# Performance work log

Hardware: AMD Instinct MI355X
Metric: run time of the kernel (lower is better)

Reference implementation:

```python
import jax, jax.numpy as jnp
import numpy as np

def _dct_mat():
    k = np.arange(8)[:, None]
    n = np.arange(8)[None, :]
    norm = np.where(k == 0, np.sqrt(1.0 / 8.0), np.sqrt(2.0 / 8.0))
    return jnp.asarray(norm * np.cos(np.pi / 8.0 * (n + 0.5) * k), jnp.float32)

_LUM = np.array([[16,11,10,16,24,40,51,61],[12,12,14,19,26,58,60,55],[14,13,16,24,40,57,69,56],[14,17,22,29,51,87,80,62],[18,22,37,56,68,109,103,77],[24,35,55,64,81,104,113,92],[49,64,78,87,103,121,120,101],[72,92,95,98,112,100,103,99]], np.float32)
_CHROM = np.array([[17,18,24,47,99,99,99,99],[18,21,26,66,99,99,99,99],[24,26,56,99,99,99,99,99],[47,66,99,99,99,99,99,99],[99,99,99,99,99,99,99,99],[99,99,99,99,99,99,99,99],[99,99,99,99,99,99,99,99],[99,99,99,99,99,99,99,99]], np.float32)

def _qtables(quality):
    q = max(1, min(100, int(quality)))
    scale = 5000.0 / q if q < 50 else 200.0 - 2.0 * q
    tbs = np.stack([_LUM, _CHROM]) * scale
    tbs = np.clip((tbs + 50.0) / 100.0, 1.0, 255.0)
    return jnp.asarray(tbs, jnp.float32)

def _jpeg_forward(img, quality):
    bs, _, oh, ow = img.shape
    x = img * 255.0
    pad_h = (8 - oh % 8) % 8
    pad_w = (8 - ow % 8) % 8
    if pad_h or pad_w:
        x = jnp.pad(x, ((0, 0), (0, 0), (0, pad_h), (0, pad_w)), mode='edge')
    h, w = oh + pad_h, ow + pad_w
    W_ycc = jnp.asarray([[0.299, 0.587, 0.114], [-0.1687, -0.3313, 0.5], [0.5, -0.4187, -0.0813]], jnp.float32)
    b_ycc = jnp.asarray([0.0, 128.0, 128.0], jnp.float32)
    # 1x1 conv colorspace transform
    yuv = jnp.einsum('oc,bchw->bohw', W_ycc, x) + b_ycc[None, :, None, None]
    nb = bs * 3
    hb, wb = h // 8, w // 8
    # unfold(kernel=8, stride=8) == non-overlapping 8x8 blocking, block-row-major
    blocks = yuv.reshape(nb, hb, 8, wb, 8).transpose(0, 1, 3, 2, 4).reshape(nb, hb * wb, 8, 8)
    M = _dct_mat()
    dct = jnp.matmul(M, jnp.matmul(blocks - 128.0, M.T))
    qt = _qtables(quality)
    # faithful to original slicing patches_dct[:bs] / [bs:] over the flattened (b,c) dim
    row = jnp.arange(nb)[:, None, None, None]
    qfull = jnp.where(row < bs, qt[0], qt[1])
    t = dct / qfull
    # straight-through round
    tq = (t + jax.lax.stop_gradient(jnp.round(t) - t)) * qfull
    idct = jnp.matmul(M.T, jnp.matmul(tq, M)) + 128.0
    rec = idct.reshape(nb, hb, wb, 8, 8).transpose(0, 1, 3, 2, 4).reshape(bs, 3, h, w)
    rec = rec - b_ycc[None, :, None, None]
    y, cb, cr = rec[:, 0], rec[:, 1], rec[:, 2]
    r = y + 1.402 * cr
    g = y - 0.34414 * cb - 0.71414 * cr
    b = y + 1.772 * cb
    rgb = jnp.stack([r, g, b], axis=1)[:, :, :oh, :ow]
    return jnp.clip(rgb / 255.0, 0.0, 1.0)

def setup_inputs() -> dict:
    key = jax.random.key(0)
    img = jax.random.uniform(key, (16, 3, 512, 512), dtype=jnp.float32)
    return {"img": img, "quality": 80}

def reference(img, quality):
    return _jpeg_forward(img, quality)
```

## Files before the change

kernel.cpp:

```cpp
#include <hip/hip_runtime.h>
#include <math.h>

#define C1 0.9807852804032304
#define C2 0.9238795325112867
#define C3 0.8314696123025452
#define C4 0.7071067811865476
#define C5 0.5555702330196022
#define C6 0.3826834323650898
#define C7 0.19509032201612825
#define N0 0.35355339059327373

static constexpr double Mc[8][8] = {
 {  N0,      N0,      N0,      N0,      N0,      N0,      N0,      N0    },
 {  .5*C1,   .5*C3,   .5*C5,   .5*C7,  -.5*C7,  -.5*C5,  -.5*C3,  -.5*C1 },
 {  .5*C2,   .5*C6,  -.5*C6,  -.5*C2,  -.5*C2,  -.5*C6,   .5*C6,   .5*C2 },
 {  .5*C3,  -.5*C7,  -.5*C1,  -.5*C5,   .5*C5,   .5*C1,   .5*C7,  -.5*C3 },
 {  .5*C4,  -.5*C4,  -.5*C4,   .5*C4,   .5*C4,  -.5*C4,  -.5*C4,   .5*C4 },
 {  .5*C5,  -.5*C1,   .5*C7,   .5*C3,  -.5*C3,  -.5*C7,   .5*C1,  -.5*C5 },
 {  .5*C6,  -.5*C2,   .5*C2,  -.5*C6,  -.5*C6,   .5*C2,  -.5*C2,   .5*C6 },
 {  .5*C7,  -.5*C5,   .5*C3,  -.5*C1,   .5*C1,  -.5*C3,   .5*C5,  -.5*C7 },
};
#define ROWF(r) {(float)Mc[r][0],(float)Mc[r][1],(float)Mc[r][2],(float)Mc[r][3],\
                 (float)Mc[r][4],(float)Mc[r][5],(float)Mc[r][6],(float)Mc[r][7]}
static constexpr float Mcf[8][8] = {ROWF(0),ROWF(1),ROWF(2),ROWF(3),ROWF(4),ROWF(5),ROWF(6),ROWF(7)};

static __device__ const double LUM_BASE[64] = {
 16,11,10,16,24,40,51,61,
 12,12,14,19,26,58,60,55,
 14,13,16,24,40,57,69,56,
 14,17,22,29,51,87,80,62,
 18,22,37,56,68,109,103,77,
 24,35,55,64,81,104,113,92,
 49,64,78,87,103,121,120,101,
 72,92,95,98,112,100,103,99};
static __device__ const double CHROM_BASE[64] = {
 17,18,24,47,99,99,99,99,
 18,21,26,66,99,99,99,99,
 24,26,56,99,99,99,99,99,
 47,66,99,99,99,99,99,99,
 99,99,99,99,99,99,99,99,
 99,99,99,99,99,99,99,99,
 99,99,99,99,99,99,99,99,
 99,99,99,99,99,99,99,99};

__global__ __launch_bounds__(192, 4) void jpeg_fwd(const float* __restrict__ img,
                                                   const int* __restrict__ quality,
                                                   float* __restrict__ out)
{
    __shared__ double QT[128];
    __shared__ double U[1728];

    const int t   = threadIdx.x;
    const int w   = t >> 6;
    const int l   = t & 63;
    const int blk = l >> 3;
    const int rr  = l & 7;

    const int b    = blockIdx.x >> 9;
    const int rem  = blockIdx.x & 511;
    const int row0 = (rem >> 3) << 3;
    const int col0 = (rem & 7) << 6;

    const size_t plane = 512 * 512;

    const float* p = img + (size_t)(b * 3) * plane + (size_t)(row0 + rr) * 512 + col0 + blk * 8;
    float4 R0 = *(const float4*)(p);
    float4 R1 = *(const float4*)(p + 4);
    float4 G0 = *(const float4*)(p + plane);
    float4 G1 = *(const float4*)(p + plane + 4);
    float4 B0 = *(const float4*)(p + 2 * plane);
    float4 B1 = *(const float4*)(p + 2 * plane + 4);

    {
        int q = quality[0];
        q = q < 1 ? 1 : (q > 100 ? 100 : q);
        double scale = (q < 50) ? (5000.0 / (double)q) : (200.0 - 2.0 * (double)q);
        #pragma unroll
        for (int h = 0; h < 2; ++h) {
            int e = l + (h << 6);
            int tbl = e >> 6, idx = e & 63;
            double base = tbl ? CHROM_BASE[idx] : LUM_BASE[idx];
            double v = (base * scale + 50.0) / 100.0;
            QT[e] = fmin(fmax(v, 1.0), 255.0);
        }
    }

    const double W00 =  0.299,   W01 =  0.587,   W02 =  0.114;
    const double W10 = -0.1687,  W11 = -0.3313,  W12 =  0.5;
    const double W20 =  0.5,     W21 = -0.4187,  W22 = -0.0813;

    float rf[8] = {R0.x, R0.y, R0.z, R0.w, R1.x, R1.y, R1.z, R1.w};
    float gf[8] = {G0.x, G0.y, G0.z, G0.w, G1.x, G1.y, G1.z, G1.w};
    float bf[8] = {B0.x, B0.y, B0.z, B0.w, B1.x, B1.y, B1.z, B1.w};

    double row[8];
    #pragma unroll
    for (int k = 0; k < 8; ++k) {
        double rv = (double)rf[k] * 255.0;
        double gv = (double)gf[k] * 255.0;
        double bv = (double)bf[k] * 255.0;
        double v;
        if (w == 0)      v = W00 * rv + W01 * gv + W02 * bv;
        else if (w == 1) v = W10 * rv + W11 * gv + W12 * bv + 128.0;
        else             v = W20 * rv + W21 * gv + W22 * bv + 128.0;
        row[k] = v - 128.0;
    }

    double y[8];
    #pragma unroll
    for (int c = 0; c < 8; ++c) {
        double s = 0.0;
        #pragma unroll
        for (int k = 0; k < 8; ++k)
            s += row[k] * Mc[c][k];
        y[c] = s;
    }

    {
        double* tb = U + w * 576 + blk * 72 + rr * 9;
        #pragma unroll
        for (int k = 0; k < 8; ++k) tb[k] = y[k];
    }
    double t1[8], qv[8];
    {
        const double* tb = U + w * 576 + blk * 72 + rr;
        #pragma unroll
        for (int k = 0; k < 8; ++k) t1[k] = tb[k * 9];
    }
    const int sel = ((b * 3 + w) < 16) ? 0 : 1;
    #pragma unroll
    for (int j = 0; j < 8; ++j) qv[j] = QT[(sel << 6) + (j << 3) + rr];

    double wq[8];
    #pragma unroll
    for (int j = 0; j < 8; ++j) {
        double s = 0.0;
        #pragma unroll
        for (int k = 0; k < 8; ++k)
            s += t1[k] * Mc[j][k];
        wq[j] = rint(s / qv[j]) * qv[j];
    }

    float wqf[8];
    #pragma unroll
    for (int k = 0; k < 8; ++k) wqf[k] = (float)wq[k];

    float a3[8];
    #pragma unroll
    for (int j = 0; j < 8; ++j) {
        float s = 0.0f;
        #pragma unroll
        for (int k = 0; k < 8; ++k)
            s += wqf[k] * Mcf[k][j];
        a3[j] = s;
    }

    {
        float* tb = (float*)(U + w * 576) + blk * 72 + rr * 9;
        #pragma unroll
        for (int k = 0; k < 8; ++k) tb[k] = a3[k];
    }
    __syncthreads();

    float tY[8], tU[8], tV[8];
    {
        const float* c0 = (float*)(U + 0 * 576) + blk * 72 + rr;
        const float* c1 = (float*)(U + 1 * 576) + blk * 72 + rr;
        const float* c2 = (float*)(U + 2 * 576) + blk * 72 + rr;
        #pragma unroll
        for (int k = 0; k < 8; ++k) {
            tY[k] = c0[k * 9];
            tU[k] = c1[k * 9];
            tV[k] = c2[k * 9];
        }
    }

    float yr[8], ur[8], vr[8];
    #pragma unroll
    for (int j = 0; j < 8; ++j) {
        float sy = 0.0f, su = 0.0f, sv = 0.0f;
        #pragma unroll
        for (int k = 0; k < 8; ++k) {
            sy += tY[k] * Mcf[k][j];
            su += tU[k] * Mcf[k][j];
            sv += tV[k] * Mcf[k][j];
        }
        yr[j] = sy; ur[j] = su; vr[j] = sv;
    }

    float* q0 = out + (size_t)(b * 3 + w) * plane + (size_t)(row0 + rr) * 512 + col0 + blk * 8;
    float o[8];
    #pragma unroll
    for (int k = 0; k < 8; ++k) {
        float yd = yr[k] + 128.0f;
        float v;
        if (w == 0)      v = yd + 1.402f * vr[k];
        else if (w == 1) v = yd - 0.34414f * ur[k] - 0.71414f * vr[k];
        else             v = yd + 1.772f * ur[k];
        o[k] = fminf(fmaxf(v * (1.0f / 255.0f), 0.0f), 1.0f);
    }
    *(float4*)(q0)     = make_float4(o[0], o[1], o[2], o[3]);
    *(float4*)(q0 + 4) = make_float4(o[4], o[5], o[6], o[7]);
}

extern "C" void kernel_launch(void* const* d_in, const int* in_sizes, int n_in,
                              void* d_out, int out_size, void* d_ws, size_t ws_size,
                              hipStream_t stream) {
    const float* img     = (const float*)d_in[0];
    const int*   quality = (const int*)d_in[1];
    float*       out     = (float*)d_out;
    jpeg_fwd<<<8192, 192, 0, stream>>>(img, quality, out);
}
```

Before: 113.0 us.

## Use even/odd DCT symmetry, reciprocal-based quantization, and fold 255 scale

Exploits the even/odd symmetry of the DCT basis to halve the multiply-adds in both forward and inverse 1D transforms. Replaces the FP64 division during quantization with a precomputed reciprocal table plus one FMA correction step. Folds the 255 scaling into the color conversion weights. FP64 arithmetic is the main compute cost, so fewer FP64 ops and no divides should lower ALU time. The risk is small rounding differences at quantization boundaries.

```diff
diff --git a/kernel.cpp b/kernel.cpp
--- a/kernel.cpp
+++ b/kernel.cpp
@@ -48,6 +48,7 @@
                                                    float* __restrict__ out)
 {
     __shared__ double QT[128];
+    __shared__ double RQ[128];
     __shared__ double U[1728];
 
     const int t   = threadIdx.x;
@@ -81,13 +82,15 @@
             int tbl = e >> 6, idx = e & 63;
             double base = tbl ? CHROM_BASE[idx] : LUM_BASE[idx];
             double v = (base * scale + 50.0) / 100.0;
-            QT[e] = fmin(fmax(v, 1.0), 255.0);
-        }
-    }
-
-    const double W00 =  0.299,   W01 =  0.587,   W02 =  0.114;
-    const double W10 = -0.1687,  W11 = -0.3313,  W12 =  0.5;
-    const double W20 =  0.5,     W21 = -0.4187,  W22 = -0.0813;
+            v = fmin(fmax(v, 1.0), 255.0);
+            QT[e] = v;
+            RQ[e] = 1.0 / v;
+        }
+    }
+
+    const double F00 =  0.299 * 255.0,  F01 =  0.587 * 255.0,  F02 =  0.114 * 255.0;
+    const double F10 = -0.1687 * 255.0, F11 = -0.3313 * 255.0, F12 =  0.5 * 255.0;
+    const double F20 =  0.5 * 255.0,    F21 = -0.4187 * 255.0, F22 = -0.0813 * 255.0;
 
     float rf[8] = {R0.x, R0.y, R0.z, R0.w, R1.x, R1.y, R1.z, R1.w};
     float gf[8] = {G0.x, G0.y, G0.z, G0.w, G1.x, G1.y, G1.z, G1.w};
@@ -96,24 +99,34 @@
     double row[8];
     #pragma unroll
     for (int k = 0; k < 8; ++k) {
-        double rv = (double)rf[k] * 255.0;
-        double gv = (double)gf[k] * 255.0;
-        double bv = (double)bf[k] * 255.0;
+        double rv = (double)rf[k];
+        double gv = (double)gf[k];
+        double bv = (double)bf[k];
         double v;
-        if (w == 0)      v = W00 * rv + W01 * gv + W02 * bv;
-        else if (w == 1) v = W10 * rv + W11 * gv + W12 * bv + 128.0;
-        else             v = W20 * rv + W21 * gv + W22 * bv + 128.0;
+        if (w == 0)      v = F00 * rv + F01 * gv + F02 * bv;
+        else if (w == 1) v = F10 * rv + F11 * gv + F12 * bv + 128.0;
+        else             v = F20 * rv + F21 * gv + F22 * bv + 128.0;
         row[k] = v - 128.0;
     }
 
     double y[8];
-    #pragma unroll
-    for (int c = 0; c < 8; ++c) {
-        double s = 0.0;
-        #pragma unroll
-        for (int k = 0; k < 8; ++k)
-            s += row[k] * Mc[c][k];
-        y[c] = s;
+    {
+        double u0[4], v0[4];
+        #pragma unroll
+        for (int k = 0; k < 4; ++k) {
+            u0[k] = row[k] + row[7 - k];
+            v0[k] = row[k] - row[7 - k];
+        }
+        #pragma unroll
+        for (int c = 0; c < 8; c += 2) {
+            double se = 0.0, so = 0.0;
+            #pragma unroll
+            for (int k = 0; k < 4; ++k) {
+                se += u0[k] * Mc[c][k];
+                so += v0[k] * Mc[c + 1][k];
+            }
+            y[c] = se; y[c + 1] = so;
+        }
     }
 
     {
@@ -121,7 +134,7 @@
         #pragma unroll
         for (int k = 0; k < 8; ++k) tb[k] = y[k];
     }
-    double t1[8], qv[8];
+    double t1[8], qv[8], rv8[8];
     {
         const double* tb = U + w * 576 + blk * 72 + rr;
         #pragma unroll
@@ -129,16 +142,42 @@
     }
     const int sel = ((b * 3 + w) < 16) ? 0 : 1;
     #pragma unroll
-    for (int j = 0; j < 8; ++j) qv[j] = QT[(sel << 6) + (j << 3) + rr];
+    for (int j = 0; j < 8; ++j) {
+        qv[j]  = QT[(sel << 6) + (j << 3) + rr];
+        rv8[j] = RQ[(sel << 6) + (j << 3) + rr];
+    }
 
     double wq[8];
-    #pragma unroll
-    for (int j = 0; j < 8; ++j) {
-        double s = 0.0;
-        #pragma unroll
-        for (int k = 0; k < 8; ++k)
-            s += t1[k] * Mc[j][k];
-        wq[j] = rint(s / qv[j]) * qv[j];
+    {
+        double tu[4], tv[4];
+        #pragma unroll
+        for (int k = 0; k < 4; ++k) {
+            tu[k] = t1[k] + t1[7 - k];
+            tv[k] = t1[k] - t1[7 - k];
+        }
+        #pragma unroll
+        for (int j = 0; j < 8; j += 2) {
+            double se = 0.0, so = 0.0;
+            #pragma unroll
+            for (int k = 0; k < 4; ++k) {
+                se += tu[k] * Mc[j][k];
+                so += tv[k] * Mc[j + 1][k];
+            }
+            {
+                double q = qv[j], r = rv8[j];
+                double qh = se * r;
+                double e  = fma(-q, qh, se);
+                double qq = fma(e, r, qh);
+                wq[j] = rint(qq) * q;
+            }
+            {
+                double q = qv[j + 1], r = rv8[j + 1];
+                double qh = so * r;
+                double e  = fma(-q, qh, so);
+                double qq = fma(e, r, qh);
+                wq[j + 1] = rint(qq) * q;
+            }
+        }
     }
 
     float wqf[8];
@@ -147,12 +186,15 @@
 
     float a3[8];
     #pragma unroll
-    for (int j = 0; j < 8; ++j) {
-        float s = 0.0f;
-        #pragma unroll
-        for (int k = 0; k < 8; ++k)
-            s += wqf[k] * Mcf[k][j];
-        a3[j] = s;
+    for (int j = 0; j < 4; ++j) {
+        float pe = 0.0f, po = 0.0f;
+        #pragma unroll
+        for (int k = 0; k < 4; ++k) {
+            pe += wqf[2 * k]     * Mcf[2 * k][j];
+            po += wqf[2 * k + 1] * Mcf[2 * k + 1][j];
+        }
+        a3[j]     = pe + po;
+        a3[7 - j] = pe - po;
     }
 
     {
@@ -177,15 +219,18 @@
 
     float yr[8], ur[8], vr[8];
     #pragma unroll
-    for (int j = 0; j < 8; ++j) {
-        float sy = 0.0f, su = 0.0f, sv = 0.0f;
-        #pragma unroll
-        for (int k = 0; k < 8; ++k) {
-            sy += tY[k] * Mcf[k][j];
-            su += tU[k] * Mcf[k][j];
-            sv += tV[k] * Mcf[k][j];
-        }
-        yr[j] = sy; ur[j] = su; vr[j] = sv;
+    for (int j = 0; j < 4; ++j) {
+        float eY = 0.0f, oY = 0.0f, eU = 0.0f, oU = 0.0f, eV = 0.0f, oV = 0.0f;
+        #pragma unroll
+        for (int k = 0; k < 4; ++k) {
+            float me = Mcf[2 * k][j], mo = Mcf[2 * k + 1][j];
+            eY += tY[2 * k] * me;  oY += tY[2 * k + 1] * mo;
+            eU += tU[2 * k] * me;  oU += tU[2 * k + 1] * mo;
+            eV += tV[2 * k] * me;  oV += tV[2 * k + 1] * mo;
+        }
+        yr[j] = eY + oY;  yr[7 - j] = eY - oY;
+        ur[j] = eU + oU;  ur[7 - j] = eU - oU;
+        vr[j] = eV + oV;  vr[7 - j] = eV - oV;
     }
 
     float* q0 = out + (size_t)(b * 3 + w) * plane + (size_t)(row0 + rr) * 512 + col0 + blk * 8;
```

After: 111.1 us. About the same (-1.7%).
